# Kernel optimization log

Measured on AMD Instinct MI355X. Metric: run time of the kernel, lower is better.

## Reference

```python
import jax, jax.numpy as jnp
import numpy as np

N, K, E, H, I = 8192, 2, 8, 2048, 1408


def setup_inputs() -> dict:
    key = jax.random.key(0)
    k1, k2, k3, k4, k5 = jax.random.split(key, 5)
    x = jax.random.normal(k1, (N, H), dtype=jnp.float32)
    topk_indices = jax.random.randint(k2, (N, K), 0, E, dtype=jnp.int32)
    topk_weights = jax.random.uniform(k3, (N, K), dtype=jnp.float32)
    # normalize routing weights per token (typical top-k softmax output scale)
    topk_weights = topk_weights / jnp.sum(topk_weights, axis=-1, keepdims=True)
    scale = 0.02  # typical init std, keeps activations well-scaled
    gate_up_proj = jax.random.normal(k4, (E, H, 2 * I), dtype=jnp.float32) * scale
    down_proj = jax.random.normal(k5, (E, I, H), dtype=jnp.float32) * scale
    return {"x": x, "topk_indices": topk_indices, "topk_weights": topk_weights,
            "gate_up_proj": gate_up_proj, "down_proj": down_proj}


def reference(x, topk_indices, topk_weights, gate_up_proj, down_proj):
    """MoE experts: route -> grouped GEMM SwiGLU -> grouped GEMM -> weighted unroute.

    x: [N, H]; topk_indices/topk_weights: [N, K];
    gate_up_proj: [E, H, 2I]; down_proj: [E, I, H].
    """
    n, k = topk_indices.shape
    e = gate_up_proj.shape[0]
    flat_e = topk_indices.reshape(-1)                 # [N*K] expert id per routed slot
    sort_idx = jnp.argsort(flat_e)                    # stable sort: group slots by expert
    token_idx = sort_idx // k                         # source token for each sorted slot
    sorted_tokens = x[token_idx]                      # [N*K, H]
    group_sizes = jnp.bincount(flat_e, length=e).astype(jnp.int32)  # [E]
    # grouped (ragged) GEMM over contiguous expert groups
    h = jax.lax.ragged_dot(sorted_tokens, gate_up_proj, group_sizes)  # [N*K, 2I]
    gate_h, up_h = jnp.split(h, 2, axis=-1)
    intermediate = jax.nn.silu(gate_h) * up_h          # fused SwiGLU
    out_sorted = jax.lax.ragged_dot(intermediate, down_proj, group_sizes)  # [N*K, H]
    # weighted scatter-combine back to token order
    w_sorted = topk_weights.reshape(-1)[sort_idx]      # [N*K]
    out = jnp.zeros_like(x).at[token_idx].add(out_sorted * w_sorted[:, None])
    return out
```

## Files before the change

kernel.cpp:

```cpp
#include <hip/hip_runtime.h>


#define N_TOK 8192
#define TOPK  2
#define NEXP  8
#define HD    2048
#define ID    1408
#define NK    (N_TOK * TOPK)

typedef __bf16 bf16x8 __attribute__((ext_vector_type(8)));
typedef float  f32x4  __attribute__((ext_vector_type(4)));

__device__ __forceinline__ float b2f(unsigned short u) {
    union { unsigned int i; float f; } v; v.i = ((unsigned int)u) << 16; return v.f;
}
__device__ __forceinline__ unsigned short f2b(float f) {
    union { float f; unsigned int i; } v; v.f = f;
    unsigned int x = v.i;
    return (unsigned short)((x + 0x7fffu + ((x >> 16) & 1u)) >> 16);
}

__device__ __forceinline__ void glds16(const void* g, void* l) {
    __builtin_amdgcn_global_load_lds(
        (const __attribute__((address_space(1))) unsigned int*)g,
        (__attribute__((address_space(3))) unsigned int*)l,
        16, 0, 0);
}


__global__ void probe_k(const unsigned short* __restrict__ xu, int* __restrict__ mode) {
    __shared__ int c;
    if (threadIdx.x == 0) c = 0;
    __syncthreads();
    float a = fabsf(b2f(xu[threadIdx.x * 2]));
    int sane = (a > 1e-4f && a < 100.f) ? 1 : 0;
    atomicAdd(&c, sane);
    __syncthreads();
    if (threadIdx.x == 0) mode[0] = (c < 512) ? 1 : 0;
}


__global__ void convert_x(const void* __restrict__ x, unsigned short* __restrict__ xb,
                          const int* __restrict__ mode) {
    int gid = blockIdx.x * 256 + threadIdx.x;
    size_t o = (size_t)gid * 8;
    if (mode[0]) {
        const float* f = (const float*)x + o;
        float4 f0 = *(const float4*)f;
        float4 f1 = *(const float4*)(f + 4);
        uint4 v;
        v.x = f2b(f0.x) | ((unsigned int)f2b(f0.y) << 16);
        v.y = f2b(f0.z) | ((unsigned int)f2b(f0.w) << 16);
        v.z = f2b(f1.x) | ((unsigned int)f2b(f1.y) << 16);
        v.w = f2b(f1.z) | ((unsigned int)f2b(f1.w) << 16);
        *(uint4*)(xb + o) = v;
    } else {
        *(uint4*)(xb + o) = *(const uint4*)((const unsigned short*)x + o);
    }
}


__global__ void init_k(int* cnt, int* fill) {
    int t = threadIdx.x;
    if (t < NEXP) { cnt[t] = 0; fill[t] = 0; }
}

__global__ void route_count(const int* __restrict__ idx, int* __restrict__ cnt) {
    int s = blockIdx.x * 256 + threadIdx.x;
    if (s < NK) atomicAdd(&cnt[idx[s]], 1);
}

__global__ void route_scan(const int* __restrict__ cnt, int* __restrict__ base) {
    if (threadIdx.x == 0) {
        int acc = 0;
        for (int e = 0; e < NEXP; e++) { base[e] = acc; acc += cnt[e]; }
        base[NEXP] = acc;
    }
}

__global__ void route_scatter(const int* __restrict__ idx,
                              const int* __restrict__ base,
                              int* __restrict__ fill,
                              int* __restrict__ tok,
                              int* __restrict__ inv) {
    int s = blockIdx.x * 256 + threadIdx.x;
    if (s < NK) {
        int e = idx[s];
        int p = base[e] + atomicAdd(&fill[e], 1);
        tok[p] = s >> 1;
        inv[s] = p;
    }
}


__global__ void transpose_k(const void* __restrict__ in, unsigned short* __restrict__ out,
                            int R, int C, const int* __restrict__ mode) {
    __shared__ float tile[64][65];
    bool fp32m = (mode[0] != 0);
    int e  = blockIdx.z;
    int c0 = blockIdx.x * 64, r0 = blockIdx.y * 64;
    int t = threadIdx.x;
    if (fp32m) {
        const float* inp = (const float*)in + (size_t)e * R * C;
        for (int i = 0; i < 16; i++) {
            int lin = t + i * 256;
            int r = lin >> 6, c = lin & 63;
            tile[r][c] = inp[(size_t)(r0 + r) * C + c0 + c];
        }
    } else {
        const unsigned int* inp = (const unsigned int*)in + (size_t)e * R * (C >> 1);
        for (int i = 0; i < 8; i++) {
            int lin = t + i * 256;
            int r = lin >> 5, cu = lin & 31;
            unsigned int v = inp[(size_t)(r0 + r) * (C >> 1) + (c0 >> 1) + cu];
            tile[r][2 * cu]     = b2f((unsigned short)(v & 0xffffu));
            tile[r][2 * cu + 1] = b2f((unsigned short)(v >> 16));
        }
    }
    __syncthreads();
    unsigned int* outp = (unsigned int*)out + (size_t)e * C * (R >> 1);
    for (int i = 0; i < 8; i++) {
        int lin = t + i * 256;
        int c = lin >> 5, ru = lin & 31;
        unsigned int lo = f2b(tile[2 * ru][c]);
        unsigned int hi = f2b(tile[2 * ru + 1][c]);
        outp[(size_t)(c0 + c) * (R >> 1) + (r0 >> 1) + ru] = lo | (hi << 16);
    }
}



__launch_bounds__(256, 2)
__global__ void gemm1_k(const unsigned short* __restrict__ xb,
                        const unsigned short* __restrict__ gupT,
                        const int* __restrict__ base,
                        const int* __restrict__ tok,
                        unsigned short* __restrict__ inter) {
    int e  = blockIdx.z;
    int rt = blockIdx.x;
    int ct = blockIdx.y;
    int rbeg = base[e], rend = base[e + 1];
    int row0 = rbeg + rt * 128;
    if (row0 >= rend) return;

    __shared__ unsigned short As[128 * 64];
    __shared__ unsigned short Bgs[128 * 64];
    __shared__ unsigned short Bus[128 * 64];

    int tid  = threadIdx.x;
    int lane = tid & 63;
    int wave = tid >> 6;
    int wm = wave & 1, wn = wave >> 1;
    int l15 = lane & 15, q = lane >> 4;

    const unsigned short* gptr = gupT + (size_t)e * (2 * ID) * HD + (size_t)(ct * 128) * HD;
    const unsigned short* uptr = gptr + (size_t)ID * HD;

    const unsigned short* agp[4];
    int boff[4];
    int wslot[4];
    for (int i = 0; i < 4; i++) {
        int s = i * 256 + wave * 64 + lane;
        int r = s >> 3;
        int c = (s & 7) ^ (r & 7);
        int p = row0 + r;
        bool sv = (p < rend);
        agp[i]  = (sv ? xb + (size_t)tok[p] * HD : xb) + c * 8;
        boff[i] = r * HD + c * 8;
        wslot[i] = (i * 256 + wave * 64) * 8;
    }

    int arow[4], brow[4];
    for (int mt = 0; mt < 4; mt++) arow[mt] = wm * 64 + mt * 16 + l15;
    for (int nt = 0; nt < 4; nt++) brow[nt] = wn * 64 + nt * 16 + l15;

    f32x4 accg[4][4], accu[4][4];
    for (int mt = 0; mt < 4; mt++)
        for (int nt = 0; nt < 4; nt++) {
            accg[mt][nt] = (f32x4){0.f, 0.f, 0.f, 0.f};
            accu[mt][nt] = (f32x4){0.f, 0.f, 0.f, 0.f};
        }

    for (int k0 = 0; k0 < HD; k0 += 64) {
        __syncthreads();
        for (int i = 0; i < 4; i++) {
            glds16(agp[i] + k0,         &As[wslot[i]]);
            glds16(gptr + boff[i] + k0, &Bgs[wslot[i]]);
            glds16(uptr + boff[i] + k0, &Bus[wslot[i]]);
        }
        __syncthreads();
        for (int ks = 0; ks < 2; ks++) {
            int kc = ks * 4 + q;
            bf16x8 af[4], bg[4], bu[4];
            for (int mt = 0; mt < 4; mt++)
                af[mt] = *(bf16x8*)&As[(arow[mt] * 8 + (kc ^ (arow[mt] & 7))) * 8];
            for (int nt = 0; nt < 4; nt++) {
                bg[nt] = *(bf16x8*)&Bgs[(brow[nt] * 8 + (kc ^ (brow[nt] & 7))) * 8];
                bu[nt] = *(bf16x8*)&Bus[(brow[nt] * 8 + (kc ^ (brow[nt] & 7))) * 8];
            }
            for (int mt = 0; mt < 4; mt++)
                for (int nt = 0; nt < 4; nt++) {
                    accg[mt][nt] = __builtin_amdgcn_mfma_f32_16x16x32_bf16(af[mt], bg[nt], accg[mt][nt], 0, 0, 0);
                    accu[mt][nt] = __builtin_amdgcn_mfma_f32_16x16x32_bf16(af[mt], bu[nt], accu[mt][nt], 0, 0, 0);
                }
        }
    }

    for (int mt = 0; mt < 4; mt++) {
        int rb = wm * 64 + mt * 16 + q * 4;
        for (int reg = 0; reg < 4; reg++) {
            int p = row0 + rb + reg;
            if (p >= rend) continue;
            for (int nt = 0; nt < 4; nt++) {
                int col = ct * 128 + wn * 64 + nt * 16 + l15;
                float g = accg[mt][nt][reg];
                float u = accu[mt][nt][reg];
                float s = g / (1.f + __expf(-g));
                inter[(size_t)p * ID + col] = f2b(s * u);
            }
        }
    }
}


__launch_bounds__(256, 3)
__global__ void gemm2_k(const unsigned short* __restrict__ inter,
                        const unsigned short* __restrict__ dwnT,
                        const int* __restrict__ base,
                        unsigned short* __restrict__ outs) {
    int e  = blockIdx.z;
    int rt = blockIdx.x;
    int ct = blockIdx.y;
    int rbeg = base[e], rend = base[e + 1];
    int row0 = rbeg + rt * 128;
    if (row0 >= rend) return;

    __shared__ unsigned short As[128 * 64];
    __shared__ unsigned short Bs[128 * 64];

    int tid  = threadIdx.x;
    int lane = tid & 63;
    int wave = tid >> 6;
    int wm = wave & 1, wn = wave >> 1;
    int l15 = lane & 15, q = lane >> 4;

    const unsigned short* bptr = dwnT + (size_t)e * HD * ID + (size_t)(ct * 128) * ID;

    const unsigned short* agp[4];
    int boff[4];
    int wslot[4];
    for (int i = 0; i < 4; i++) {
        int s = i * 256 + wave * 64 + lane;
        int r = s >> 3;
        int c = (s & 7) ^ (r & 7);
        int p = row0 + r;
        bool sv = (p < rend);
        agp[i]  = (sv ? inter + (size_t)p * ID : inter) + c * 8;
        boff[i] = r * ID + c * 8;
        wslot[i] = (i * 256 + wave * 64) * 8;
    }

    int arow[4], brow[4];
    for (int mt = 0; mt < 4; mt++) arow[mt] = wm * 64 + mt * 16 + l15;
    for (int nt = 0; nt < 4; nt++) brow[nt] = wn * 64 + nt * 16 + l15;

    f32x4 acc[4][4];
    for (int mt = 0; mt < 4; mt++)
        for (int nt = 0; nt < 4; nt++) acc[mt][nt] = (f32x4){0.f, 0.f, 0.f, 0.f};

    for (int k0 = 0; k0 < ID; k0 += 64) {
        __syncthreads();
        for (int i = 0; i < 4; i++) {
            glds16(agp[i] + k0,         &As[wslot[i]]);
            glds16(bptr + boff[i] + k0, &Bs[wslot[i]]);
        }
        __syncthreads();
        for (int ks = 0; ks < 2; ks++) {
            int kc = ks * 4 + q;
            bf16x8 af[4], bf[4];
            for (int mt = 0; mt < 4; mt++)
                af[mt] = *(bf16x8*)&As[(arow[mt] * 8 + (kc ^ (arow[mt] & 7))) * 8];
            for (int nt = 0; nt < 4; nt++)
                bf[nt] = *(bf16x8*)&Bs[(brow[nt] * 8 + (kc ^ (brow[nt] & 7))) * 8];
            for (int mt = 0; mt < 4; mt++)
                for (int nt = 0; nt < 4; nt++)
                    acc[mt][nt] = __builtin_amdgcn_mfma_f32_16x16x32_bf16(af[mt], bf[nt], acc[mt][nt], 0, 0, 0);
        }
    }

    for (int mt = 0; mt < 4; mt++) {
        int rb = wm * 64 + mt * 16 + q * 4;
        for (int reg = 0; reg < 4; reg++) {
            int p = row0 + rb + reg;
            if (p >= rend) continue;
            for (int nt = 0; nt < 4; nt++) {
                int col = ct * 128 + wn * 64 + nt * 16 + l15;
                outs[(size_t)p * HD + col] = f2b(acc[mt][nt][reg]);
            }
        }
    }
}


__global__ void combine_k(const unsigned short* __restrict__ outs,
                          const int* __restrict__ inv,
                          const void* __restrict__ w,
                          void* __restrict__ out,
                          const int* __restrict__ mode) {
    bool fp32m = (mode[0] != 0);
    int gid = blockIdx.x * 256 + threadIdx.x;
    int t  = gid >> 8;
    int c8 = (gid & 255) * 8;
    int p0 = inv[t * 2], p1 = inv[t * 2 + 1];
    float w0, w1;
    if (fp32m) {
        const float* wf = (const float*)w;
        w0 = wf[t * 2]; w1 = wf[t * 2 + 1];
    } else {
        const unsigned short* wu = (const unsigned short*)w;
        w0 = b2f(wu[t * 2]); w1 = b2f(wu[t * 2 + 1]);
    }
    uint4 v0 = *(const uint4*)(outs + (size_t)p0 * HD + c8);
    uint4 v1 = *(const uint4*)(outs + (size_t)p1 * HD + c8);
    const unsigned short* a = (const unsigned short*)&v0;
    const unsigned short* b = (const unsigned short*)&v1;
    float r[8];
    for (int i = 0; i < 8; i++) r[i] = w0 * b2f(a[i]) + w1 * b2f(b[i]);
    if (fp32m) {
        float* of = (float*)out + (size_t)t * HD + c8;
        *(float4*)of       = make_float4(r[0], r[1], r[2], r[3]);
        *(float4*)(of + 4) = make_float4(r[4], r[5], r[6], r[7]);
    } else {
        uint4 o;
        unsigned int* ro = (unsigned int*)&o;
        for (int i = 0; i < 4; i++)
            ro[i] = f2b(r[2 * i]) | ((unsigned int)f2b(r[2 * i + 1]) << 16);
        *(uint4*)((unsigned short*)out + (size_t)t * HD + c8) = o;
    }
}


extern "C" void kernel_launch(void* const* d_in, const int* in_sizes, int n_in,
                              void* d_out, int out_size, void* d_ws, size_t ws_size,
                              hipStream_t stream) {
    const void* x   = d_in[0];
    const int*  idx = (const int*)d_in[1];
    const void* w   = d_in[2];
    const void* gup = d_in[3];
    const void* dwn = d_in[4];

    char* ws = (char*)d_ws;
    int* mode = (int*)(ws);
    int* cnt  = (int*)(ws + 64);
    int* base = (int*)(ws + 128);
    int* fill = (int*)(ws + 192);
    int* tok  = (int*)(ws + 256);
    int* inv  = (int*)(ws + 256 + 4 * NK);
    unsigned short* inter = (unsigned short*)(ws + 262144);
    unsigned short* outs  = inter + (size_t)NK * ID;
    unsigned short* gupT  = outs  + (size_t)NK * HD;
    unsigned short* dwnT  = gupT  + (size_t)NEXP * 2 * ID * HD;
    unsigned short* xb    = dwnT  + (size_t)NEXP * HD * ID;

    probe_k<<<1, 1024, 0, stream>>>((const unsigned short*)x, mode);
    convert_x<<<(N_TOK * HD / 8) / 256, 256, 0, stream>>>(x, xb, mode);

    init_k<<<1, 64, 0, stream>>>(cnt, fill);
    route_count<<<NK / 256, 256, 0, stream>>>(idx, cnt);
    route_scan<<<1, 64, 0, stream>>>(cnt, base);
    route_scatter<<<NK / 256, 256, 0, stream>>>(idx, base, fill, tok, inv);

    transpose_k<<<dim3(2 * ID / 64, HD / 64, NEXP), 256, 0, stream>>>(
        gup, gupT, HD, 2 * ID, mode);
    transpose_k<<<dim3(HD / 64, ID / 64, NEXP), 256, 0, stream>>>(
        dwn, dwnT, ID, HD, mode);

    gemm1_k<<<dim3(128, ID / 128, NEXP), 256, 0, stream>>>(xb, gupT, base, tok, inter);
    gemm2_k<<<dim3(128, HD / 128, NEXP), 256, 0, stream>>>(inter, dwnT, base, outs);

    combine_k<<<(N_TOK * HD / 8) / 256, 256, 0, stream>>>(outs, inv, w, d_out, mode);
}
```

Measured before the change: 1.085 ms.

## Unify grouped GEMMs with double-buffered LDS, compact tile grid, XCD remap, split SwiGLU

The two grouped GEMMs become one templated kernel that loads the next K-slice into a second LDS buffer while the current one is multiplied, so the compute loop needs one barrier per iteration instead of two. The 3D grid that launched many empty row tiles is replaced by a flat grid over per-expert tile prefix sums, and block ids are remapped so consecutive work groups land on the same XCD. Gate and up projections are now computed as one GEMM over 2I columns, with SwiGLU moved into a separate elementwise kernel that runs in place. The cost is an extra round trip through memory for the 2I-wide intermediate, an extra launch, and the second GEMM reading A with a stride of 2I. Its output also reuses the gup transpose buffer.

```diff
diff --git a/kernel.cpp b/kernel.cpp
--- a/kernel.cpp
+++ b/kernel.cpp
@@ -7,6 +7,7 @@
 #define HD    2048
 #define ID    1408
 #define NK    (N_TOK * TOPK)
+#define MAXRT 136
 
 typedef __bf16 bf16x8 __attribute__((ext_vector_type(8)));
 typedef float  f32x4  __attribute__((ext_vector_type(4)));
@@ -70,11 +71,15 @@
     if (s < NK) atomicAdd(&cnt[idx[s]], 1);
 }
 
-__global__ void route_scan(const int* __restrict__ cnt, int* __restrict__ base) {
+__global__ void route_scan(const int* __restrict__ cnt, int* __restrict__ base,
+                           int* __restrict__ tb) {
     if (threadIdx.x == 0) {
-        int acc = 0;
-        for (int e = 0; e < NEXP; e++) { base[e] = acc; acc += cnt[e]; }
-        base[NEXP] = acc;
+        int acc = 0, tacc = 0;
+        for (int e = 0; e < NEXP; e++) {
+            base[e] = acc; tb[e] = tacc;
+            acc += cnt[e]; tacc += (cnt[e] + 127) >> 7;
+        }
+        base[NEXP] = acc; tb[NEXP] = tacc;
     }
 }
 
@@ -130,31 +135,37 @@
 
 
 
+template<int KD, int ND, int LDA, bool GATHER>
 __launch_bounds__(256, 2)
-__global__ void gemm1_k(const unsigned short* __restrict__ xb,
-                        const unsigned short* __restrict__ gupT,
-                        const int* __restrict__ base,
-                        const int* __restrict__ tok,
-                        unsigned short* __restrict__ inter) {
-    int e  = blockIdx.z;
-    int rt = blockIdx.x;
-    int ct = blockIdx.y;
-    int rbeg = base[e], rend = base[e + 1];
-    int row0 = rbeg + rt * 128;
-    if (row0 >= rend) return;
-
-    __shared__ unsigned short As[128 * 64];
-    __shared__ unsigned short Bgs[128 * 64];
-    __shared__ unsigned short Bus[128 * 64];
+__global__ void gemm_k(const unsigned short* __restrict__ A,
+                       const unsigned short* __restrict__ B,
+                       const int* __restrict__ base,
+                       const int* __restrict__ tb,
+                       const int* __restrict__ tok,
+                       unsigned short* __restrict__ C) {
+    const int CT = ND / 128;
+    int G = gridDim.x;
+    int orig = blockIdx.x;
+    int q8 = G >> 3, r8 = G & 7, xcd = orig & 7, lin = orig >> 3;
+    int wgid = (xcd < r8 ? xcd * (q8 + 1) : r8 * (q8 + 1) + (xcd - r8) * q8) + lin;
+    int ct  = wgid % CT;
+    int rtf = wgid / CT;
+    if (rtf >= tb[NEXP]) return;
+    int e = 0;
+    while (tb[e + 1] <= rtf) e++;
+    int row0 = base[e] + (rtf - tb[e]) * 128;
+    int rend = base[e + 1];
+
+    __shared__ unsigned short As[2][128 * 64];
+    __shared__ unsigned short Bs[2][128 * 64];
 
     int tid  = threadIdx.x;
     int lane = tid & 63;
     int wave = tid >> 6;
     int wm = wave & 1, wn = wave >> 1;
-    int l15 = lane & 15, q = lane >> 4;
-
-    const unsigned short* gptr = gupT + (size_t)e * (2 * ID) * HD + (size_t)(ct * 128) * HD;
-    const unsigned short* uptr = gptr + (size_t)ID * HD;
+    int l15 = lane & 15, qq = lane >> 4;
+
+    const unsigned short* bptr = B + (size_t)e * ND * KD + (size_t)(ct * 128) * KD;
 
     const unsigned short* agp[4];
     int boff[4];
@@ -165,140 +176,91 @@
         int c = (s & 7) ^ (r & 7);
         int p = row0 + r;
         bool sv = (p < rend);
-        agp[i]  = (sv ? xb + (size_t)tok[p] * HD : xb) + c * 8;
-        boff[i] = r * HD + c * 8;
+        const unsigned short* arow;
+        if (GATHER) arow = sv ? A + (size_t)tok[p] * LDA : A;
+        else        arow = sv ? A + (size_t)p * LDA      : A;
+        agp[i]  = arow + c * 8;
+        boff[i] = r * KD + c * 8;
         wslot[i] = (i * 256 + wave * 64) * 8;
     }
 
-    int arow[4], brow[4];
-    for (int mt = 0; mt < 4; mt++) arow[mt] = wm * 64 + mt * 16 + l15;
-    for (int nt = 0; nt < 4; nt++) brow[nt] = wn * 64 + nt * 16 + l15;
-
-    f32x4 accg[4][4], accu[4][4];
+    int arow_[4], brow_[4];
+    for (int mt = 0; mt < 4; mt++) arow_[mt] = wm * 64 + mt * 16 + l15;
+    for (int nt = 0; nt < 4; nt++) brow_[nt] = wn * 64 + nt * 16 + l15;
+
+    f32x4 acc[4][4];
     for (int mt = 0; mt < 4; mt++)
-        for (int nt = 0; nt < 4; nt++) {
-            accg[mt][nt] = (f32x4){0.f, 0.f, 0.f, 0.f};
-            accu[mt][nt] = (f32x4){0.f, 0.f, 0.f, 0.f};
-        }
-
-    for (int k0 = 0; k0 < HD; k0 += 64) {
-        __syncthreads();
-        for (int i = 0; i < 4; i++) {
-            glds16(agp[i] + k0,         &As[wslot[i]]);
-            glds16(gptr + boff[i] + k0, &Bgs[wslot[i]]);
-            glds16(uptr + boff[i] + k0, &Bus[wslot[i]]);
-        }
-        __syncthreads();
+        for (int nt = 0; nt < 4; nt++) acc[mt][nt] = (f32x4){0.f, 0.f, 0.f, 0.f};
+
+#define STAGE(buf, kk)                                          \
+    for (int i = 0; i < 4; i++) {                               \
+        glds16(agp[i] + (kk),            &As[buf][wslot[i]]);   \
+        glds16(bptr + boff[i] + (kk),    &Bs[buf][wslot[i]]);   \
+    }
+
+    STAGE(0, 0);
+    __builtin_amdgcn_sched_barrier(0);
+    asm volatile("s_waitcnt vmcnt(0)" ::: "memory");
+    __builtin_amdgcn_s_barrier();
+    __builtin_amdgcn_sched_barrier(0);
+
+    int cur = 0;
+    for (int k0 = 0; k0 < KD; k0 += 64) {
+        if (k0 + 64 < KD) { STAGE(cur ^ 1, k0 + 64); }
         for (int ks = 0; ks < 2; ks++) {
-            int kc = ks * 4 + q;
-            bf16x8 af[4], bg[4], bu[4];
+            int kc = ks * 4 + qq;
+            bf16x8 af[4], bq[4];
             for (int mt = 0; mt < 4; mt++)
-                af[mt] = *(bf16x8*)&As[(arow[mt] * 8 + (kc ^ (arow[mt] & 7))) * 8];
-            for (int nt = 0; nt < 4; nt++) {
-                bg[nt] = *(bf16x8*)&Bgs[(brow[nt] * 8 + (kc ^ (brow[nt] & 7))) * 8];
-                bu[nt] = *(bf16x8*)&Bus[(brow[nt] * 8 + (kc ^ (brow[nt] & 7))) * 8];
-            }
+                af[mt] = *(bf16x8*)&As[cur][(arow_[mt] * 8 + (kc ^ (arow_[mt] & 7))) * 8];
+            for (int nt = 0; nt < 4; nt++)
+                bq[nt] = *(bf16x8*)&Bs[cur][(brow_[nt] * 8 + (kc ^ (brow_[nt] & 7))) * 8];
             for (int mt = 0; mt < 4; mt++)
-                for (int nt = 0; nt < 4; nt++) {
-                    accg[mt][nt] = __builtin_amdgcn_mfma_f32_16x16x32_bf16(af[mt], bg[nt], accg[mt][nt], 0, 0, 0);
-                    accu[mt][nt] = __builtin_amdgcn_mfma_f32_16x16x32_bf16(af[mt], bu[nt], accu[mt][nt], 0, 0, 0);
-                }
-        }
-    }
+                for (int nt = 0; nt < 4; nt++)
+                    acc[mt][nt] = __builtin_amdgcn_mfma_f32_16x16x32_bf16(
+                        af[mt], bq[nt], acc[mt][nt], 0, 0, 0);
+        }
+        __builtin_amdgcn_sched_barrier(0);
+        asm volatile("s_waitcnt vmcnt(0)" ::: "memory");
+        __builtin_amdgcn_s_barrier();
+        __builtin_amdgcn_sched_barrier(0);
+        cur ^= 1;
+    }
+#undef STAGE
 
     for (int mt = 0; mt < 4; mt++) {
-        int rb = wm * 64 + mt * 16 + q * 4;
+        int rb = wm * 64 + mt * 16 + qq * 4;
         for (int reg = 0; reg < 4; reg++) {
             int p = row0 + rb + reg;
             if (p >= rend) continue;
             for (int nt = 0; nt < 4; nt++) {
                 int col = ct * 128 + wn * 64 + nt * 16 + l15;
-                float g = accg[mt][nt][reg];
-                float u = accu[mt][nt][reg];
-                float s = g / (1.f + __expf(-g));
-                inter[(size_t)p * ID + col] = f2b(s * u);
+                C[(size_t)p * ND + col] = f2b(acc[mt][nt][reg]);
             }
         }
     }
 }
 
 
-__launch_bounds__(256, 3)
-__global__ void gemm2_k(const unsigned short* __restrict__ inter,
-                        const unsigned short* __restrict__ dwnT,
-                        const int* __restrict__ base,
-                        unsigned short* __restrict__ outs) {
-    int e  = blockIdx.z;
-    int rt = blockIdx.x;
-    int ct = blockIdx.y;
-    int rbeg = base[e], rend = base[e + 1];
-    int row0 = rbeg + rt * 128;
-    if (row0 >= rend) return;
-
-    __shared__ unsigned short As[128 * 64];
-    __shared__ unsigned short Bs[128 * 64];
-
-    int tid  = threadIdx.x;
-    int lane = tid & 63;
-    int wave = tid >> 6;
-    int wm = wave & 1, wn = wave >> 1;
-    int l15 = lane & 15, q = lane >> 4;
-
-    const unsigned short* bptr = dwnT + (size_t)e * HD * ID + (size_t)(ct * 128) * ID;
-
-    const unsigned short* agp[4];
-    int boff[4];
-    int wslot[4];
+__global__ void swiglu_k(unsigned short* __restrict__ h) {
+    int gid = blockIdx.x * 256 + threadIdx.x;
+    int row = gid >> 8;
+    row = gid / (ID / 8);
+    int c8 = (gid - row * (ID / 8)) * 8;
+    unsigned short* hr = h + (size_t)row * (2 * ID);
+    uint4 gv = *(const uint4*)(hr + c8);
+    uint4 uv = *(const uint4*)(hr + ID + c8);
+    const unsigned short* ga = (const unsigned short*)&gv;
+    const unsigned short* ua = (const unsigned short*)&uv;
+    uint4 o;
+    unsigned int* ro = (unsigned int*)&o;
     for (int i = 0; i < 4; i++) {
-        int s = i * 256 + wave * 64 + lane;
-        int r = s >> 3;
-        int c = (s & 7) ^ (r & 7);
-        int p = row0 + r;
-        bool sv = (p < rend);
-        agp[i]  = (sv ? inter + (size_t)p * ID : inter) + c * 8;
-        boff[i] = r * ID + c * 8;
-        wslot[i] = (i * 256 + wave * 64) * 8;
-    }
-
-    int arow[4], brow[4];
-    for (int mt = 0; mt < 4; mt++) arow[mt] = wm * 64 + mt * 16 + l15;
-    for (int nt = 0; nt < 4; nt++) brow[nt] = wn * 64 + nt * 16 + l15;
-
-    f32x4 acc[4][4];
-    for (int mt = 0; mt < 4; mt++)
-        for (int nt = 0; nt < 4; nt++) acc[mt][nt] = (f32x4){0.f, 0.f, 0.f, 0.f};
-
-    for (int k0 = 0; k0 < ID; k0 += 64) {
-        __syncthreads();
-        for (int i = 0; i < 4; i++) {
-            glds16(agp[i] + k0,         &As[wslot[i]]);
-            glds16(bptr + boff[i] + k0, &Bs[wslot[i]]);
-        }
-        __syncthreads();
-        for (int ks = 0; ks < 2; ks++) {
-            int kc = ks * 4 + q;
-            bf16x8 af[4], bf[4];
-            for (int mt = 0; mt < 4; mt++)
-                af[mt] = *(bf16x8*)&As[(arow[mt] * 8 + (kc ^ (arow[mt] & 7))) * 8];
-            for (int nt = 0; nt < 4; nt++)
-                bf[nt] = *(bf16x8*)&Bs[(brow[nt] * 8 + (kc ^ (brow[nt] & 7))) * 8];
-            for (int mt = 0; mt < 4; mt++)
-                for (int nt = 0; nt < 4; nt++)
-                    acc[mt][nt] = __builtin_amdgcn_mfma_f32_16x16x32_bf16(af[mt], bf[nt], acc[mt][nt], 0, 0, 0);
-        }
-    }
-
-    for (int mt = 0; mt < 4; mt++) {
-        int rb = wm * 64 + mt * 16 + q * 4;
-        for (int reg = 0; reg < 4; reg++) {
-            int p = row0 + rb + reg;
-            if (p >= rend) continue;
-            for (int nt = 0; nt < 4; nt++) {
-                int col = ct * 128 + wn * 64 + nt * 16 + l15;
-                outs[(size_t)p * HD + col] = f2b(acc[mt][nt][reg]);
-            }
-        }
-    }
+        float g0 = b2f(ga[2 * i]),     u0 = b2f(ua[2 * i]);
+        float g1 = b2f(ga[2 * i + 1]), u1 = b2f(ua[2 * i + 1]);
+        float s0 = (g0 / (1.f + __expf(-g0))) * u0;
+        float s1 = (g1 / (1.f + __expf(-g1))) * u1;
+        ro[i] = f2b(s0) | ((unsigned int)f2b(s1) << 16);
+    }
+    *(uint4*)(hr + c8) = o;
 }
 
 
@@ -354,20 +316,21 @@
     int* cnt  = (int*)(ws + 64);
     int* base = (int*)(ws + 128);
     int* fill = (int*)(ws + 192);
-    int* tok  = (int*)(ws + 256);
-    int* inv  = (int*)(ws + 256 + 4 * NK);
-    unsigned short* inter = (unsigned short*)(ws + 262144);
-    unsigned short* outs  = inter + (size_t)NK * ID;
-    unsigned short* gupT  = outs  + (size_t)NK * HD;
-    unsigned short* dwnT  = gupT  + (size_t)NEXP * 2 * ID * HD;
-    unsigned short* xb    = dwnT  + (size_t)NEXP * HD * ID;
+    int* tb   = (int*)(ws + 256);
+    int* tok  = (int*)(ws + 512);
+    int* inv  = (int*)(ws + 512 + 4 * NK);
+    unsigned short* h    = (unsigned short*)(ws + 262144);
+    unsigned short* xb   = h    + (size_t)NK * 2 * ID;
+    unsigned short* dwnT = xb   + (size_t)N_TOK * HD;
+    unsigned short* gupT = dwnT + (size_t)NEXP * HD * ID;
+    unsigned short* outs = gupT;
 
     probe_k<<<1, 1024, 0, stream>>>((const unsigned short*)x, mode);
     convert_x<<<(N_TOK * HD / 8) / 256, 256, 0, stream>>>(x, xb, mode);
 
     init_k<<<1, 64, 0, stream>>>(cnt, fill);
     route_count<<<NK / 256, 256, 0, stream>>>(idx, cnt);
-    route_scan<<<1, 64, 0, stream>>>(cnt, base);
+    route_scan<<<1, 64, 0, stream>>>(cnt, base, tb);
     route_scatter<<<NK / 256, 256, 0, stream>>>(idx, base, fill, tok, inv);
 
     transpose_k<<<dim3(2 * ID / 64, HD / 64, NEXP), 256, 0, stream>>>(
@@ -375,8 +338,11 @@
     transpose_k<<<dim3(HD / 64, ID / 64, NEXP), 256, 0, stream>>>(
         dwn, dwnT, ID, HD, mode);
 
-    gemm1_k<<<dim3(128, ID / 128, NEXP), 256, 0, stream>>>(xb, gupT, base, tok, inter);
-    gemm2_k<<<dim3(128, HD / 128, NEXP), 256, 0, stream>>>(inter, dwnT, base, outs);
+    gemm_k<HD, 2 * ID, HD, true><<<MAXRT * (2 * ID / 128), 256, 0, stream>>>(
+        xb, gupT, base, tb, tok, h);
+    swiglu_k<<<(NK * (ID / 8)) / 256, 256, 0, stream>>>(h);
+    gemm_k<ID, HD, 2 * ID, false><<<MAXRT * (HD / 128), 256, 0, stream>>>(
+        h, dwnT, base, tb, tok, outs);
 
     combine_k<<<(N_TOK * HD / 8) / 256, 256, 0, stream>>>(outs, inv, w, d_out, mode);
 }
```

Result: faster. 989.3 us (-8.8%).
